# Kernel optimization log

Hardware: AMD Instinct MI355X
Metric: run time of the kernel (lower is better)

Reference implementation:

```python
import jax, jax.numpy as jnp
import numpy as np

D_MODEL = 1024
N_HEADS = 16
D_HEAD = D_MODEL // N_HEADS
B, S = 4, 2048


def setup_inputs() -> dict:
    key = jax.random.key(0)
    ks = jax.random.split(key, 8)
    scale = 1.0 / np.sqrt(D_MODEL)
    x = jax.random.normal(ks[0], (B, S, D_MODEL), dtype=jnp.float32)
    relative_bias = jax.random.normal(ks[1], (1, N_HEADS, S, S), dtype=jnp.float32)
    w_q = jax.random.normal(ks[2], (D_MODEL, D_MODEL), dtype=jnp.float32) * scale
    w_k = jax.random.normal(ks[3], (D_MODEL, D_MODEL), dtype=jnp.float32) * scale
    w_v = jax.random.normal(ks[4], (D_MODEL, D_MODEL), dtype=jnp.float32) * scale
    w_o = jax.random.normal(ks[5], (D_MODEL, D_MODEL), dtype=jnp.float32) * scale
    b_o = jax.random.normal(ks[6], (D_MODEL,), dtype=jnp.float32) * 0.02
    return {"x": x, "relative_bias": relative_bias, "w_q": w_q, "w_k": w_k,
            "w_v": w_v, "w_o": w_o, "b_o": b_o}


def reference(x, relative_bias, w_q, w_k, w_v, w_o, b_o):
    b, s, d = x.shape
    # torch nn.Linear computes x @ W^T; weights stored [out, in]
    def proj(w):
        y = jnp.einsum('bsd,ed->bse', x, w)  # [B,S,D]
        return y.reshape(b, s, N_HEADS, D_HEAD).transpose(0, 2, 1, 3)  # [B,H,S,Dh]
    q, k, v = proj(w_q), proj(w_k), proj(w_v)
    scores = jnp.einsum('bhqd,bhkd->bhqk', q, k) / jnp.sqrt(
        jnp.asarray(D_HEAD, x.dtype)) + relative_bias
    attn = jax.nn.softmax(scores, axis=-1)
    ctx = jnp.einsum('bhqk,bhkd->bhqd', attn, v)
    ctx = ctx.transpose(0, 2, 1, 3).reshape(b, s, d)
    return jnp.einsum('bsd,ed->bse', ctx, w_o) + b_o
```

## Files before the change

kernel.cpp:

```cpp
#include <hip/hip_runtime.h>
#include <hip/hip_bf16.h>

#define D_MODEL 1024
#define N_HEADS 16
#define D_HEAD  64
#define BATCH   4
#define SEQ     2048
#define LOG2E   1.44269504088896f

typedef __attribute__((ext_vector_type(8))) short short8;
typedef __attribute__((ext_vector_type(8))) unsigned short ushort8;
typedef __attribute__((ext_vector_type(4))) unsigned short ushort4v;
typedef __attribute__((ext_vector_type(4))) float f32x4;

__device__ inline unsigned short f2bf(float f) {
  unsigned int u = __builtin_bit_cast(unsigned int, f);
  u += 0x7fffu + ((u >> 16) & 1u);
  return (unsigned short)(u >> 16);
}

__device__ inline float exp2_fast(float x) {
  return __builtin_amdgcn_exp2f(x);
}

__device__ inline f32x4 mfma_bf16(short8 a, short8 b, f32x4 c) {
  return __builtin_amdgcn_mfma_f32_16x16x32_bf16(a, b, c, 0, 0, 0);
}

__global__ void cvt_kernel(const float* __restrict__ src,
                           unsigned short* __restrict__ dst, int n) {
  int i = (blockIdx.x * 256 + threadIdx.x) * 8;
  if (i >= n) return;
  float4 a = *reinterpret_cast<const float4*>(src + i);
  float4 b = *reinterpret_cast<const float4*>(src + i + 4);
  ushort8 o;
  o[0] = f2bf(a.x); o[1] = f2bf(a.y); o[2] = f2bf(a.z); o[3] = f2bf(a.w);
  o[4] = f2bf(b.x); o[5] = f2bf(b.y); o[6] = f2bf(b.z); o[7] = f2bf(b.w);
  *reinterpret_cast<ushort8*>(dst + i) = o;
}

template<int NBYTES>
__device__ inline void stage_swz(const unsigned short* g0, int g_stride_elems,
                                 unsigned short* lds0, int tid) {
#pragma unroll
  for (int it = 0; it < NBYTES / 4096; ++it) {
    int o = it * 4096 + tid * 16;
    int r = o >> 7;
    int cb = (o & 127) ^ ((r & 7) << 4);
    unsigned short* g = const_cast<unsigned short*>(g0) +
                        (size_t)r * g_stride_elems + (cb >> 1);
    unsigned short* l = lds0 + (o >> 1);
    __builtin_amdgcn_global_load_lds((__attribute__((address_space(1))) void*)g,
                                     (__attribute__((address_space(3))) void*)l,
                                     16, 0, 0);
  }
}

__device__ inline short8 frag_ld(const unsigned short* tile, int row, int col_el) {
  int cb = (col_el << 1) ^ ((row & 7) << 4);
  return *reinterpret_cast<const short8*>(
      reinterpret_cast<const char*>(tile) + row * 128 + cb);
}

__launch_bounds__(256, 2)
__global__ void qkv_gemm(const unsigned short* __restrict__ xb,
                         const unsigned short* __restrict__ wb,
                         unsigned short* __restrict__ Qo,
                         unsigned short* __restrict__ Ko,
                         unsigned short* __restrict__ Vt) {
  __shared__ __align__(16) unsigned short As[128][64];
  __shared__ __align__(16) unsigned short Bs[128][64];
  const int z = blockIdx.z;
  const int m0 = blockIdx.y * 128;
  const int n0 = blockIdx.x * 128;
  const int tid = threadIdx.x;
  const int lane = tid & 63;
  const int wv = tid >> 6;
  const int wr = wv >> 1, wc = wv & 1;
  const int lrow = lane & 15;
  const int lk8 = (lane >> 4) << 3;
  const unsigned short* w = wb + (size_t)z * D_MODEL * D_MODEL;

  f32x4 acc[4][4];
  const f32x4 zero = {0.f, 0.f, 0.f, 0.f};
#pragma unroll
  for (int i = 0; i < 4; ++i)
#pragma unroll
    for (int j = 0; j < 4; ++j) acc[i][j] = zero;

  for (int k0 = 0; k0 < D_MODEL; k0 += 64) {
    __syncthreads();
    stage_swz<16384>(xb + (size_t)m0 * D_MODEL + k0, D_MODEL, &As[0][0], tid);
    stage_swz<16384>(w  + (size_t)n0 * D_MODEL + k0, D_MODEL, &Bs[0][0], tid);
    __syncthreads();
#pragma unroll
    for (int ks = 0; ks < 2; ++ks) {
      short8 af[4], bfr[4];
#pragma unroll
      for (int mi = 0; mi < 4; ++mi)
        af[mi] = frag_ld(&As[0][0], wr * 64 + mi * 16 + lrow, ks * 32 + lk8);
#pragma unroll
      for (int ni = 0; ni < 4; ++ni)
        bfr[ni] = frag_ld(&Bs[0][0], wc * 64 + ni * 16 + lrow, ks * 32 + lk8);
      if (z != 2) {
#pragma unroll
        for (int mi = 0; mi < 4; ++mi)
#pragma unroll
          for (int ni = 0; ni < 4; ++ni)
            acc[mi][ni] = mfma_bf16(af[mi], bfr[ni], acc[mi][ni]);
      } else {
#pragma unroll
        for (int ni = 0; ni < 4; ++ni)
#pragma unroll
          for (int mi = 0; mi < 4; ++mi)
            acc[ni][mi] = mfma_bf16(bfr[ni], af[mi], acc[ni][mi]);
      }
    }
  }

  const int lrr = (lane >> 4) << 2;
  if (z != 2) {
    unsigned short* dst = (z == 0) ? Qo : Ko;
    const float scale = (z == 0) ? 0.125f * LOG2E : 1.0f;
#pragma unroll
    for (int mi = 0; mi < 4; ++mi)
#pragma unroll
      for (int ni = 0; ni < 4; ++ni)
#pragma unroll
        for (int r = 0; r < 4; ++r) {
          int m = m0 + wr * 64 + mi * 16 + lrr + r;
          int e = n0 + wc * 64 + ni * 16 + lrow;
          int b = m >> 11, s = m & (SEQ - 1);
          int h = e >> 6, dh = e & 63;
          dst[((size_t)(b * N_HEADS + h) * SEQ + s) * D_HEAD + dh] =
              f2bf(acc[mi][ni][r] * scale);
        }
  } else {
#pragma unroll
    for (int ni = 0; ni < 4; ++ni)
#pragma unroll
      for (int mi = 0; mi < 4; ++mi)
#pragma unroll
        for (int r = 0; r < 4; ++r) {
          int e = n0 + wc * 64 + ni * 16 + lrr + r;
          int m = m0 + wr * 64 + mi * 16 + lrow;
          int b = m >> 11, s = m & (SEQ - 1);
          int h = e >> 6, dh = e & 63;
          Vt[((size_t)(b * N_HEADS + h) * D_HEAD + dh) * SEQ + s] =
              f2bf(acc[ni][mi][r]);
        }
  }
}

__launch_bounds__(256, 3)
__global__ void attn_kernel(const unsigned short* __restrict__ Q,
                            const unsigned short* __restrict__ K,
                            const unsigned short* __restrict__ Vt,
                            const float* __restrict__ bias,
                            unsigned short* __restrict__ ctx) {
  __shared__ __align__(16) unsigned short Qs[64][64];
  __shared__ __align__(16) unsigned short Ks[2][64][64];
  __shared__ __align__(16) unsigned short Vs[2][64][64];
  __shared__ __align__(16) unsigned short Ps[4][16][72];

  const int lid = blockIdx.x + 32 * blockIdx.y + 512 * blockIdx.z;
  const int xg = lid & 7, g = lid >> 3;
  const int bg = g & 1;
  const int h = (xg << 1) | ((g >> 1) & 1);
  const int q0 = ((g >> 2) & 31) << 6;

  const int tid = threadIdx.x, lane = tid & 63, wv = tid >> 6;
  const int lrow = lane & 15;
  const int lgrp = lane >> 4;
  const int lk8 = lgrp << 3;
  const int lrr = lgrp << 2;

  short8 qf[2][2];
#pragma unroll
  for (int b = 0; b < 2; ++b) {
    const int bb = bg * 2 + b;
    stage_swz<8192>(Q + ((size_t)(bb * N_HEADS + h) * SEQ + q0) * D_HEAD,
                    D_HEAD, &Qs[0][0], tid);
    __syncthreads();
#pragma unroll
    for (int ks = 0; ks < 2; ++ks)
      qf[b][ks] = frag_ld(&Qs[0][0], wv * 16 + lrow, ks * 32 + lk8);
    __syncthreads();
  }

  stage_swz<8192>(K + (size_t)(bg * 2 * N_HEADS + h) * SEQ * D_HEAD, D_HEAD,
                  &Ks[0][0][0], tid);
  stage_swz<8192>(Vt + (size_t)(bg * 2 * N_HEADS + h) * D_HEAD * SEQ, SEQ,
                  &Vs[0][0][0], tid);

  const float* bp = bias + (size_t)h * SEQ * SEQ +
                    (size_t)(q0 + wv * 16 + lrow) * SEQ + lrr;
  f32x4 bcur[4], bnext[4];
#pragma unroll
  for (int nt = 0; nt < 4; ++nt)
    bcur[nt] = *reinterpret_cast<const f32x4*>(bp + nt * 16) * LOG2E;

  float m_run[2], l_run[2];
  f32x4 o_acc[2][4];
  const f32x4 zero = {0.f, 0.f, 0.f, 0.f};
#pragma unroll
  for (int b = 0; b < 2; ++b) {
    m_run[b] = -1e30f; l_run[b] = 0.f;
#pragma unroll
    for (int dt = 0; dt < 4; ++dt) o_acc[b][dt] = zero;
  }

  __syncthreads();

  for (int kt = 0; kt < 32; ++kt) {
    if (kt < 31) {
#pragma unroll
      for (int nt = 0; nt < 4; ++nt)
        bnext[nt] = *reinterpret_cast<const f32x4*>(bp + (kt + 1) * 64 +
                                                    nt * 16) * LOG2E;
    }

#pragma unroll
    for (int b = 0; b < 2; ++b) {
      const int cur = b;

      if (!(kt == 31 && b == 1)) {
        const int nb = bg * 2 + (b ^ 1);
        const int nkt = kt + b;
        stage_swz<8192>(K + (size_t)(nb * N_HEADS + h) * SEQ * D_HEAD +
                            (size_t)nkt * 64 * D_HEAD,
                        D_HEAD, &Ks[cur ^ 1][0][0], tid);
        stage_swz<8192>(Vt + (size_t)(nb * N_HEADS + h) * D_HEAD * SEQ +
                            nkt * 64,
                        SEQ, &Vs[cur ^ 1][0][0], tid);
      }

      f32x4 s[4];
#pragma unroll
      for (int nt = 0; nt < 4; ++nt) s[nt] = bcur[nt];
      __builtin_amdgcn_s_setprio(1);
#pragma unroll
      for (int ks = 0; ks < 2; ++ks)
#pragma unroll
        for (int nt = 0; nt < 4; ++nt) {
          short8 kf = frag_ld(&Ks[cur][0][0], nt * 16 + lrow, ks * 32 + lk8);
          s[nt] = mfma_bf16(kf, qf[b][ks], s[nt]);
        }
      __builtin_amdgcn_s_setprio(0);

      float pmax =
          fmaxf(fmaxf(fmaxf(fmaxf(s[0][0], s[0][1]), s[0][2]),
                      fmaxf(fmaxf(s[1][0], s[1][1]), s[1][2])),
                fmaxf(fmaxf(fmaxf(s[2][0], s[2][1]), s[2][2]),
                      fmaxf(fmaxf(fmaxf(s[3][0], s[3][1]), s[3][2]),
                            fmaxf(fmaxf(s[0][3], s[1][3]),
                                  fmaxf(s[2][3], s[3][3])))));
      pmax = fmaxf(pmax, __shfl_xor(pmax, 16));
      pmax = fmaxf(pmax, __shfl_xor(pmax, 32));

      if (!__all(pmax - m_run[b] <= 11.0f)) {
        float mnew = fmaxf(m_run[b], pmax);
        float corr = exp2_fast(m_run[b] - mnew);
        l_run[b] *= corr;
        m_run[b] = mnew;
#pragma unroll
        for (int r = 0; r < 4; ++r) {
          float c = __shfl(corr, lrr + r);
#pragma unroll
          for (int dt = 0; dt < 4; ++dt) o_acc[b][dt][r] *= c;
        }
      }

      float p[4][4];
      float rs = 0.f;
#pragma unroll
      for (int nt = 0; nt < 4; ++nt)
#pragma unroll
        for (int r = 0; r < 4; ++r) {
          float e = exp2_fast(s[nt][r] - m_run[b]);
          p[nt][r] = e;
          rs += e;
        }
      rs += __shfl_xor(rs, 16);
      rs += __shfl_xor(rs, 32);
      l_run[b] += rs;

#pragma unroll
      for (int nt = 0; nt < 4; ++nt) {
        ushort4v pk;
#pragma unroll
        for (int r = 0; r < 4; ++r)
          pk[r] = __builtin_bit_cast(unsigned short,
                                     __float2bfloat16(p[nt][r]));
        *reinterpret_cast<ushort4v*>(&Ps[wv][lrow][nt * 16 + lrr]) = pk;
      }

      short8 pf[2];
#pragma unroll
      for (int ks = 0; ks < 2; ++ks)
        pf[ks] = *reinterpret_cast<const short8*>(&Ps[wv][lrow][ks * 32 + lk8]);
      __builtin_amdgcn_s_setprio(1);
#pragma unroll
      for (int ks = 0; ks < 2; ++ks)
#pragma unroll
        for (int dt = 0; dt < 4; ++dt) {
          short8 vf = frag_ld(&Vs[cur][0][0], dt * 16 + lrow, ks * 32 + lk8);
          o_acc[b][dt] = mfma_bf16(pf[ks], vf, o_acc[b][dt]);
        }
      __builtin_amdgcn_s_setprio(0);

      __syncthreads();
    }

    if (kt < 31) {
#pragma unroll
      for (int nt = 0; nt < 4; ++nt) bcur[nt] = bnext[nt];
    }
  }

#pragma unroll
  for (int b = 0; b < 2; ++b) {
    const int bb = bg * 2 + b;
    float inv = 1.0f / l_run[b];
#pragma unroll
    for (int r = 0; r < 4; ++r) {
      float invq = __shfl(inv, lrr + r);
      int qs = q0 + wv * 16 + lrr + r;
#pragma unroll
      for (int dt = 0; dt < 4; ++dt)
        ctx[((size_t)bb * SEQ + qs) * D_MODEL + h * 64 + dt * 16 + lrow] =
            f2bf(o_acc[b][dt][r] * invq);
    }
  }
}

__launch_bounds__(256, 2)
__global__ void out_gemm(const unsigned short* __restrict__ cb,
                         const unsigned short* __restrict__ wo,
                         const float* __restrict__ bo,
                         float* __restrict__ out) {
  __shared__ __align__(16) unsigned short As[128][64];
  __shared__ __align__(16) unsigned short Bs[128][64];
  const int m0 = blockIdx.y * 128;
  const int n0 = blockIdx.x * 128;
  const int tid = threadIdx.x;
  const int lane = tid & 63;
  const int wv = tid >> 6;
  const int wr = wv >> 1, wc = wv & 1;
  const int lrow = lane & 15;
  const int lk8 = (lane >> 4) << 3;

  f32x4 acc[4][4];
  const f32x4 zero = {0.f, 0.f, 0.f, 0.f};
#pragma unroll
  for (int i = 0; i < 4; ++i)
#pragma unroll
    for (int j = 0; j < 4; ++j) acc[i][j] = zero;

  for (int k0 = 0; k0 < D_MODEL; k0 += 64) {
    __syncthreads();
    stage_swz<16384>(cb + (size_t)m0 * D_MODEL + k0, D_MODEL, &As[0][0], tid);
    stage_swz<16384>(wo + (size_t)n0 * D_MODEL + k0, D_MODEL, &Bs[0][0], tid);
    __syncthreads();
#pragma unroll
    for (int ks = 0; ks < 2; ++ks) {
      short8 af[4], bfr[4];
#pragma unroll
      for (int mi = 0; mi < 4; ++mi)
        af[mi] = frag_ld(&As[0][0], wr * 64 + mi * 16 + lrow, ks * 32 + lk8);
#pragma unroll
      for (int ni = 0; ni < 4; ++ni)
        bfr[ni] = frag_ld(&Bs[0][0], wc * 64 + ni * 16 + lrow, ks * 32 + lk8);
#pragma unroll
      for (int mi = 0; mi < 4; ++mi)
#pragma unroll
        for (int ni = 0; ni < 4; ++ni)
          acc[mi][ni] = mfma_bf16(af[mi], bfr[ni], acc[mi][ni]);
    }
  }

  const int lrr = (lane >> 4) << 2;
#pragma unroll
  for (int mi = 0; mi < 4; ++mi)
#pragma unroll
    for (int ni = 0; ni < 4; ++ni)
#pragma unroll
      for (int r = 0; r < 4; ++r) {
        int m = m0 + wr * 64 + mi * 16 + lrr + r;
        int e = n0 + wc * 64 + ni * 16 + lrow;
        out[(size_t)m * D_MODEL + e] = acc[mi][ni][r] + bo[e];
      }
}

extern "C" void kernel_launch(void* const* d_in, const int* in_sizes, int n_in,
                              void* d_out, int out_size, void* d_ws, size_t ws_size,
                              hipStream_t stream) {
  const float* x    = (const float*)d_in[0];
  const float* bias = (const float*)d_in[1];
  const float* w_q  = (const float*)d_in[2];
  const float* w_k  = (const float*)d_in[3];
  const float* w_v  = (const float*)d_in[4];
  const float* w_o  = (const float*)d_in[5];
  const float* b_o  = (const float*)d_in[6];
  float* out = (float*)d_out;

  const size_t NX = (size_t)BATCH * SEQ * D_MODEL;
  const size_t NW = (size_t)D_MODEL * D_MODEL;

  unsigned short* xb    = (unsigned short*)d_ws;
  unsigned short* wqkvb = xb + NX;
  unsigned short* wob   = wqkvb + 3 * NW;
  unsigned short* Qb    = wob + NW;
  unsigned short* Kb    = Qb + NX;
  unsigned short* Vtb   = Kb + NX;
  unsigned short* ctxb  = Vtb + NX;

  cvt_kernel<<<(int)(NX / 2048), 256, 0, stream>>>(x, xb, (int)NX);
  cvt_kernel<<<(int)(NW / 2048), 256, 0, stream>>>(w_q, wqkvb, (int)NW);
  cvt_kernel<<<(int)(NW / 2048), 256, 0, stream>>>(w_k, wqkvb + NW, (int)NW);
  cvt_kernel<<<(int)(NW / 2048), 256, 0, stream>>>(w_v, wqkvb + 2 * NW, (int)NW);
  cvt_kernel<<<(int)(NW / 2048), 256, 0, stream>>>(w_o, wob, (int)NW);

  qkv_gemm<<<dim3(8, 64, 3), 256, 0, stream>>>(xb, wqkvb, Qb, Kb, Vtb);
  attn_kernel<<<dim3(32, 16, 2), 256, 0, stream>>>(Qb, Kb, Vtb, bias, ctxb);
  out_gemm<<<dim3(8, 64), 256, 0, stream>>>(ctxb, wob, b_o, out);
}
```

Baseline: 322.4 us.

## Triple-buffer K/V tiles with explicit vmcnt waits and raw barriers in attention

Moves the attention K/V shared-memory staging from double to triple buffering, reusing one buffer for the initial Q load. It replaces __syncthreads with explicit s_waitcnt vmcnt counts plus s_barrier, so that global loads for the next tile stay in flight while the current tile is computed. The loop is peeled for the last two steps, and the per-step compute is factored into a helper. Launch bounds drop from 3 to 2 blocks per SM to make room for the extra LDS and registers. The hand-set vmcnt counts depend on how many loads stage_swz issues, which is a correctness risk.

After: 319.8 us. No clear change (-0.8%).

```diff
diff --git a/kernel.cpp b/kernel.cpp
--- a/kernel.cpp
+++ b/kernel.cpp
@@ -152,15 +152,89 @@
   }
 }
 
-__launch_bounds__(256, 3)
+__device__ __forceinline__ void attn_step_compute(
+    const unsigned short* Kb, const unsigned short* Vb,
+    unsigned short (&PsW)[16][72], const f32x4 (&bcur)[4],
+    const short8 (&qfb)[2], f32x4 (&oacc)[4], float& m_run, float& l_run,
+    int lrow, int lk8, int lrr) {
+  f32x4 s[4];
+#pragma unroll
+  for (int nt = 0; nt < 4; ++nt) s[nt] = bcur[nt];
+  __builtin_amdgcn_s_setprio(1);
+#pragma unroll
+  for (int ks = 0; ks < 2; ++ks)
+#pragma unroll
+    for (int nt = 0; nt < 4; ++nt) {
+      short8 kf = frag_ld(Kb, nt * 16 + lrow, ks * 32 + lk8);
+      s[nt] = mfma_bf16(kf, qfb[ks], s[nt]);
+    }
+  __builtin_amdgcn_s_setprio(0);
+
+  float pmax =
+      fmaxf(fmaxf(fmaxf(fmaxf(s[0][0], s[0][1]), s[0][2]),
+                  fmaxf(fmaxf(s[1][0], s[1][1]), s[1][2])),
+            fmaxf(fmaxf(fmaxf(s[2][0], s[2][1]), s[2][2]),
+                  fmaxf(fmaxf(fmaxf(s[3][0], s[3][1]), s[3][2]),
+                        fmaxf(fmaxf(s[0][3], s[1][3]),
+                              fmaxf(s[2][3], s[3][3])))));
+  pmax = fmaxf(pmax, __shfl_xor(pmax, 16));
+  pmax = fmaxf(pmax, __shfl_xor(pmax, 32));
+
+  if (!__all(pmax - m_run <= 11.0f)) {
+    float mnew = fmaxf(m_run, pmax);
+    float corr = exp2_fast(m_run - mnew);
+    l_run *= corr;
+    m_run = mnew;
+#pragma unroll
+    for (int r = 0; r < 4; ++r) {
+      float c = __shfl(corr, lrr + r);
+#pragma unroll
+      for (int dt = 0; dt < 4; ++dt) oacc[dt][r] *= c;
+    }
+  }
+
+  float rs = 0.f;
+#pragma unroll
+  for (int nt = 0; nt < 4; ++nt) {
+    float p0 = exp2_fast(s[nt][0] - m_run);
+    float p1 = exp2_fast(s[nt][1] - m_run);
+    float p2 = exp2_fast(s[nt][2] - m_run);
+    float p3 = exp2_fast(s[nt][3] - m_run);
+    rs += (p0 + p1) + (p2 + p3);
+    ushort4v pk;
+    pk[0] = __builtin_bit_cast(unsigned short, __float2bfloat16(p0));
+    pk[1] = __builtin_bit_cast(unsigned short, __float2bfloat16(p1));
+    pk[2] = __builtin_bit_cast(unsigned short, __float2bfloat16(p2));
+    pk[3] = __builtin_bit_cast(unsigned short, __float2bfloat16(p3));
+    *reinterpret_cast<ushort4v*>(&PsW[lrow][nt * 16 + lrr]) = pk;
+  }
+  rs += __shfl_xor(rs, 16);
+  rs += __shfl_xor(rs, 32);
+  l_run += rs;
+
+  short8 pf[2];
+#pragma unroll
+  for (int ks = 0; ks < 2; ++ks)
+    pf[ks] = *reinterpret_cast<const short8*>(&PsW[lrow][ks * 32 + lk8]);
+  __builtin_amdgcn_s_setprio(1);
+#pragma unroll
+  for (int ks = 0; ks < 2; ++ks)
+#pragma unroll
+    for (int dt = 0; dt < 4; ++dt) {
+      short8 vf = frag_ld(Vb, dt * 16 + lrow, ks * 32 + lk8);
+      oacc[dt] = mfma_bf16(pf[ks], vf, oacc[dt]);
+    }
+  __builtin_amdgcn_s_setprio(0);
+}
+
+__launch_bounds__(256, 2)
 __global__ void attn_kernel(const unsigned short* __restrict__ Q,
                             const unsigned short* __restrict__ K,
                             const unsigned short* __restrict__ Vt,
                             const float* __restrict__ bias,
                             unsigned short* __restrict__ ctx) {
-  __shared__ __align__(16) unsigned short Qs[64][64];
-  __shared__ __align__(16) unsigned short Ks[2][64][64];
-  __shared__ __align__(16) unsigned short Vs[2][64][64];
+  __shared__ __align__(16) unsigned short Ks[3][64][64];
+  __shared__ __align__(16) unsigned short Vs[3][64][64];
   __shared__ __align__(16) unsigned short Ps[4][16][72];
 
   const int lid = blockIdx.x + 32 * blockIdx.y + 512 * blockIdx.z;
@@ -180,11 +254,11 @@
   for (int b = 0; b < 2; ++b) {
     const int bb = bg * 2 + b;
     stage_swz<8192>(Q + ((size_t)(bb * N_HEADS + h) * SEQ + q0) * D_HEAD,
-                    D_HEAD, &Qs[0][0], tid);
+                    D_HEAD, &Ks[2][0][0], tid);
     __syncthreads();
 #pragma unroll
     for (int ks = 0; ks < 2; ++ks)
-      qf[b][ks] = frag_ld(&Qs[0][0], wv * 16 + lrow, ks * 32 + lk8);
+      qf[b][ks] = frag_ld(&Ks[2][0][0], wv * 16 + lrow, ks * 32 + lk8);
     __syncthreads();
   }
 
@@ -200,6 +274,12 @@
   for (int nt = 0; nt < 4; ++nt)
     bcur[nt] = *reinterpret_cast<const f32x4*>(bp + nt * 16) * LOG2E;
 
+  stage_swz<8192>(K + (size_t)((bg * 2 + 1) * N_HEADS + h) * SEQ * D_HEAD,
+                  D_HEAD, &Ks[1][0][0], tid);
+  stage_swz<8192>(Vt + (size_t)((bg * 2 + 1) * N_HEADS + h) * D_HEAD * SEQ,
+                  SEQ, &Vs[1][0][0], tid);
+  asm volatile("" ::: "memory");
+
   float m_run[2], l_run[2];
   f32x4 o_acc[2][4];
   const f32x4 zero = {0.f, 0.f, 0.f, 0.f};
@@ -210,112 +290,59 @@
     for (int dt = 0; dt < 4; ++dt) o_acc[b][dt] = zero;
   }
 
-  __syncthreads();
-
-  for (int kt = 0; kt < 32; ++kt) {
-    if (kt < 31) {
-#pragma unroll
-      for (int nt = 0; nt < 4; ++nt)
-        bnext[nt] = *reinterpret_cast<const f32x4*>(bp + (kt + 1) * 64 +
-                                                    nt * 16) * LOG2E;
-    }
-
+  int cur = 0;
+
+  for (int kt = 0; kt < 31; ++kt) {
 #pragma unroll
     for (int b = 0; b < 2; ++b) {
-      const int cur = b;
-
-      if (!(kt == 31 && b == 1)) {
-        const int nb = bg * 2 + (b ^ 1);
-        const int nkt = kt + b;
-        stage_swz<8192>(K + (size_t)(nb * N_HEADS + h) * SEQ * D_HEAD +
-                            (size_t)nkt * 64 * D_HEAD,
-                        D_HEAD, &Ks[cur ^ 1][0][0], tid);
-        stage_swz<8192>(Vt + (size_t)(nb * N_HEADS + h) * D_HEAD * SEQ +
-                            nkt * 64,
-                        SEQ, &Vs[cur ^ 1][0][0], tid);
+      const int nxt = cur >= 1 ? cur - 1 : cur + 2;
+      stage_swz<8192>(K + (size_t)((bg * 2 + b) * N_HEADS + h) * SEQ * D_HEAD +
+                          (size_t)(kt + 1) * 64 * D_HEAD,
+                      D_HEAD, &Ks[nxt][0][0], tid);
+      stage_swz<8192>(Vt + (size_t)((bg * 2 + b) * N_HEADS + h) * D_HEAD * SEQ +
+                          (kt + 1) * 64,
+                      SEQ, &Vs[nxt][0][0], tid);
+      if (b == 0) {
+#pragma unroll
+        for (int nt = 0; nt < 4; ++nt)
+          bnext[nt] = *reinterpret_cast<const f32x4*>(bp + (kt + 1) * 64 +
+                                                      nt * 16) * LOG2E;
       }
-
-      f32x4 s[4];
-#pragma unroll
-      for (int nt = 0; nt < 4; ++nt) s[nt] = bcur[nt];
-      __builtin_amdgcn_s_setprio(1);
-#pragma unroll
-      for (int ks = 0; ks < 2; ++ks)
-#pragma unroll
-        for (int nt = 0; nt < 4; ++nt) {
-          short8 kf = frag_ld(&Ks[cur][0][0], nt * 16 + lrow, ks * 32 + lk8);
-          s[nt] = mfma_bf16(kf, qf[b][ks], s[nt]);
-        }
-      __builtin_amdgcn_s_setprio(0);
-
-      float pmax =
-          fmaxf(fmaxf(fmaxf(fmaxf(s[0][0], s[0][1]), s[0][2]),
-                      fmaxf(fmaxf(s[1][0], s[1][1]), s[1][2])),
-                fmaxf(fmaxf(fmaxf(s[2][0], s[2][1]), s[2][2]),
-                      fmaxf(fmaxf(fmaxf(s[3][0], s[3][1]), s[3][2]),
-                            fmaxf(fmaxf(s[0][3], s[1][3]),
-                                  fmaxf(s[2][3], s[3][3])))));
-      pmax = fmaxf(pmax, __shfl_xor(pmax, 16));
-      pmax = fmaxf(pmax, __shfl_xor(pmax, 32));
-
-      if (!__all(pmax - m_run[b] <= 11.0f)) {
-        float mnew = fmaxf(m_run[b], pmax);
-        float corr = exp2_fast(m_run[b] - mnew);
-        l_run[b] *= corr;
-        m_run[b] = mnew;
-#pragma unroll
-        for (int r = 0; r < 4; ++r) {
-          float c = __shfl(corr, lrr + r);
-#pragma unroll
-          for (int dt = 0; dt < 4; ++dt) o_acc[b][dt][r] *= c;
-        }
-      }
-
-      float p[4][4];
-      float rs = 0.f;
-#pragma unroll
-      for (int nt = 0; nt < 4; ++nt)
-#pragma unroll
-        for (int r = 0; r < 4; ++r) {
-          float e = exp2_fast(s[nt][r] - m_run[b]);
-          p[nt][r] = e;
-          rs += e;
-        }
-      rs += __shfl_xor(rs, 16);
-      rs += __shfl_xor(rs, 32);
-      l_run[b] += rs;
-
-#pragma unroll
-      for (int nt = 0; nt < 4; ++nt) {
-        ushort4v pk;
-#pragma unroll
-        for (int r = 0; r < 4; ++r)
-          pk[r] = __builtin_bit_cast(unsigned short,
-                                     __float2bfloat16(p[nt][r]));
-        *reinterpret_cast<ushort4v*>(&Ps[wv][lrow][nt * 16 + lrr]) = pk;
-      }
-
-      short8 pf[2];
-#pragma unroll
-      for (int ks = 0; ks < 2; ++ks)
-        pf[ks] = *reinterpret_cast<const short8*>(&Ps[wv][lrow][ks * 32 + lk8]);
-      __builtin_amdgcn_s_setprio(1);
-#pragma unroll
-      for (int ks = 0; ks < 2; ++ks)
-#pragma unroll
-        for (int dt = 0; dt < 4; ++dt) {
-          short8 vf = frag_ld(&Vs[cur][0][0], dt * 16 + lrow, ks * 32 + lk8);
-          o_acc[b][dt] = mfma_bf16(pf[ks], vf, o_acc[b][dt]);
-        }
-      __builtin_amdgcn_s_setprio(0);
-
-      __syncthreads();
-    }
-
-    if (kt < 31) {
-#pragma unroll
-      for (int nt = 0; nt < 4; ++nt) bcur[nt] = bnext[nt];
-    }
+      asm volatile("" ::: "memory");
+      asm volatile("s_waitcnt vmcnt(12)" ::: "memory");
+      __builtin_amdgcn_s_barrier();
+      asm volatile("" ::: "memory");
+
+      if (b == 0)
+        attn_step_compute(&Ks[cur][0][0], &Vs[cur][0][0], Ps[wv], bcur, qf[0],
+                          o_acc[0], m_run[0], l_run[0], lrow, lk8, lrr);
+      else
+        attn_step_compute(&Ks[cur][0][0], &Vs[cur][0][0], Ps[wv], bcur, qf[1],
+                          o_acc[1], m_run[1], l_run[1], lrow, lk8, lrr);
+
+      asm volatile("" ::: "memory");
+      __builtin_amdgcn_s_barrier();
+      cur = cur >= 2 ? 0 : cur + 1;
+    }
+#pragma unroll
+    for (int nt = 0; nt < 4; ++nt) bcur[nt] = bnext[nt];
+  }
+
+  {
+    asm volatile("s_waitcnt vmcnt(4)" ::: "memory");
+    __builtin_amdgcn_s_barrier();
+    asm volatile("" ::: "memory");
+    attn_step_compute(&Ks[cur][0][0], &Vs[cur][0][0], Ps[wv], bcur, qf[0],
+                      o_acc[0], m_run[0], l_run[0], lrow, lk8, lrr);
+    asm volatile("" ::: "memory");
+    __builtin_amdgcn_s_barrier();
+    cur = cur >= 2 ? 0 : cur + 1;
+
+    asm volatile("s_waitcnt vmcnt(0)" ::: "memory");
+    __builtin_amdgcn_s_barrier();
+    asm volatile("" ::: "memory");
+    attn_step_compute(&Ks[cur][0][0], &Vs[cur][0][0], Ps[wv], bcur, qf[1],
+                      o_acc[1], m_run[1], l_run[1], lrow, lk8, lrr);
   }
 
 #pragma unroll
```
